# Performance work log

Measured on AMD Instinct MI355X. Metric: run time of the kernel, lower is better.

## Reference

```python
import jax, jax.numpy as jnp
import numpy as np

WS = 7        # window size
IMG = 56      # input resolution (H = W)
BATCH = 32    # image batch
DIM = 384
HEADS = 12
HEAD_DIM = DIM // HEADS
N = WS * WS                      # tokens per window = 49
NW = (IMG // WS) * (IMG // WS)   # windows per image = 64
B_ = BATCH * NW                  # 2048
TBL = (2 * WS - 1) ** 2          # 169


def _rel_index(ws):
    # standard Swin relative position index, values in [0, (2ws-1)^2)
    coords = np.stack(np.meshgrid(np.arange(ws), np.arange(ws), indexing='ij'))
    coords = coords.reshape(2, -1)                       # (2, N)
    rel = coords[:, :, None] - coords[:, None, :]        # (2, N, N)
    rel = rel.transpose(1, 2, 0).astype(np.int64).copy()
    rel[:, :, 0] += ws - 1
    rel[:, :, 1] += ws - 1
    rel[:, :, 0] *= 2 * ws - 1
    return rel.sum(-1)                                   # (N, N)


def _shift_mask(H, W, ws, shift):
    # shifted-window attention mask, (nW, N, N) with 0 / -100
    img = np.zeros((H, W))
    cnt = 0
    for hs in (slice(0, -ws), slice(-ws, -shift), slice(-shift, None)):
        for wsl in (slice(0, -ws), slice(-ws, -shift), slice(-shift, None)):
            img[hs, wsl] = cnt
            cnt += 1
    win = img.reshape(H // ws, ws, W // ws, ws).transpose(0, 2, 1, 3).reshape(-1, ws * ws)
    diff = win[:, None, :] - win[:, :, None]
    return np.where(diff != 0, -100.0, 0.0).astype(np.float32)


def setup_inputs() -> dict:
    key = jax.random.key(0)
    ks = jax.random.split(key, 7)
    s = 0.02
    return {
        'x': jax.random.normal(ks[0], (B_, N, DIM), jnp.float32),
        'mask': jnp.asarray(_shift_mask(IMG, IMG, WS, WS // 2)),
        'rpe_indices': jnp.asarray(_rel_index(WS)),
        'qkv_w': jax.random.normal(ks[1], (3 * DIM, DIM), jnp.float32) * s,
        'qkv_b': jnp.zeros((3 * DIM,), jnp.float32),
        'proj_w': jax.random.normal(ks[2], (DIM, DIM), jnp.float32) * s,
        'proj_b': jnp.zeros((DIM,), jnp.float32),
        'q_rpe': jax.random.normal(ks[3], (HEADS, HEAD_DIM, TBL), jnp.float32) * s,
        'k_rpe': jax.random.normal(ks[4], (HEADS, HEAD_DIM, TBL), jnp.float32) * s,
        'v_rpe': jax.random.normal(ks[5], (HEADS, TBL, HEAD_DIM), jnp.float32) * s,
    }


def reference(x, mask, rpe_indices, qkv_w, qkv_b, proj_w, proj_b, q_rpe, k_rpe, v_rpe):
    B, n, C = x.shape
    h, hd = q_rpe.shape[0], q_rpe.shape[1]
    scale = hd ** -0.5

    qkv = x @ qkv_w.T + qkv_b                                   # (B, N, 3C)
    qkv = qkv.reshape(B, n, 3, h, hd).transpose(2, 0, 3, 1, 4)   # (3, B, h, N, hd)
    q, k, v = qkv[0] * scale, qkv[1], qkv[2]

    attn = jnp.einsum('bhid,bhjd->bhij', q, k)                   # (B, h, N, N)

    # Contextual q/k bias. The torch code does b_q.flatten(2)[:, :, rpe_indices]
    # with rpe_indices in [0, TBL): gathering from the flattened (N*TBL) axis with
    # indices < TBL selects row 0 of the N axis, i.e. b_q[:, :, 0, rpe_indices].
    # We compute only that row, which is mathematically identical.
    bq0 = jnp.einsum('bhd,hdt->bht', q[:, :, 0], q_rpe)          # (B, h, TBL)
    bk0 = jnp.einsum('bhd,hdt->bht', k[:, :, 0], k_rpe)          # (B, h, TBL)
    attn = attn + (bq0 + bk0)[:, :, rpe_indices]                 # gather -> (B, h, N, N)

    nW = mask.shape[0]
    attn = attn.reshape(B // nW, nW, h, n, n) + mask[None, :, None]
    attn = jax.nn.softmax(attn.reshape(B, h, n, n), axis=-1)

    # contextual v bias: w = v_rpe[:, rpe_indices] -> (h, N, N, hd)
    w = v_rpe[:, rpe_indices.reshape(-1)].reshape(h, n, n, hd)
    r_v = jnp.einsum('bhij,hijd->bihd', attn, w).reshape(B, n, C)

    out = jnp.einsum('bhij,bhjd->bihd', attn, v).reshape(B, n, C) + r_v
    out = out @ proj_w.T + proj_b
    return out, attn
```

## Files before the change

### kernel.cpp

```cpp
#include <hip/hip_runtime.h>


typedef unsigned int u32;
typedef unsigned short u16;
typedef __attribute__((ext_vector_type(8))) short bf16x8;
typedef __attribute__((ext_vector_type(4))) float f32x4;
typedef float f4a __attribute__((ext_vector_type(4), aligned(4)));

#define SCALE 0.17677669529663687f

__device__ __forceinline__ u16 f2b(float f) {
  union { float f; u32 u; } c; c.f = f;
  u32 u = c.u;
  return (u16)((u + 0x7FFFu + ((u >> 16) & 1u)) >> 16);
}
__device__ __forceinline__ float b2f(u16 s) {
  union { float f; u32 u; } c; c.u = ((u32)s) << 16;
  return c.f;
}
__device__ __forceinline__ u32 pk2(float lo, float hi) {
  return (u32)f2b(lo) | ((u32)f2b(hi) << 16);
}
__device__ __forceinline__ void async16(void* lds, const void* g) {
  __builtin_amdgcn_global_load_lds(
      (const __attribute__((address_space(1))) u32*)g,
      (__attribute__((address_space(3))) u32*)lds, 16, 0, 0);
}

__global__ __launch_bounds__(256) void k_prep(
    const float* __restrict__ qkv_w, const float* __restrict__ proj_w,
    const float* __restrict__ mask, const int* __restrict__ idx,
    u16* __restrict__ wqkvb, u16* __restrict__ wprojb, u16* __restrict__ mbi) {
  int bx = blockIdx.x, tid = threadIdx.x;
  if (bx < 432) {
    int i = bx * 256 + tid;
    float4 v = ((const float4*)qkv_w)[i];
    ushort4 o; o.x = f2b(v.x); o.y = f2b(v.y); o.z = f2b(v.z); o.w = f2b(v.w);
    ((ushort4*)wqkvb)[i] = o;
  } else if (bx < 576) {
    int i = (bx - 432) * 256 + tid;
    float4 v = ((const float4*)proj_w)[i];
    ushort4 o; o.x = f2b(v.x); o.y = f2b(v.y); o.z = f2b(v.z); o.w = f2b(v.w);
    ((ushort4*)wprojb)[i] = o;
  } else {
    int i = (bx - 576) * 256 + tid;
    if (i < 64 * 2401) {
      int p = i % 2401;
      mbi[i] = (u16)(idx[p] | ((mask[i] != 0.0f) ? 256 : 0));
    }
  }
}

__global__ __launch_bounds__(256) void k_qkv(
    const float* __restrict__ X, const u16* __restrict__ Bw,
    const float* __restrict__ bias, u16* __restrict__ outq) {
  int bx0 = blockIdx.x;
  int bx = (bx0 & 7) * 882 + (bx0 >> 3);
  int mt = bx / 9, nt = bx - mt * 9;
  size_t m0 = (size_t)mt * 128;
  int n0 = nt * 128;
  int tid = threadIdx.x;
  int w = tid >> 6, l = tid & 63;
  int wm = w >> 1, wn = w & 1;
  int lr = l & 15, lg = l >> 4;
  int rdo = (lg ^ ((lr >> 1) & 3)) << 3;

  __shared__ u16 At[4096];
  __shared__ u16 Bt[2][4096];

  f32x4 acc[4][4] = {};
  int row = tid >> 2;
  int c8 = (((tid & 3) ^ ((row >> 1) & 3)) << 3);
  const u16* gB  = Bw + (size_t)(n0 + row) * 384 + c8;
  const u16* gB2 = Bw + (size_t)(n0 + row + 64) * 384 + c8;
  const float* gX  = X + (m0 + row) * 384 + c8;
  const float* gX2 = X + (m0 + row + 64) * 384 + c8;

  float4 ar[2][4];
  async16(&Bt[0][tid * 8], gB);
  async16(&Bt[0][(256 + tid) * 8], gB2);
  ar[0][0] = *(const float4*)(gX);
  ar[0][1] = *(const float4*)(gX + 4);
  ar[0][2] = *(const float4*)(gX2);
  ar[0][3] = *(const float4*)(gX2 + 4);

#pragma unroll
  for (int t = 0; t < 12; ++t) {
    int cur = t & 1, nxt = cur ^ 1;
    int k1 = ((t < 11) ? (t + 1) : 11) * 32;
    async16(&Bt[nxt][tid * 8], gB + k1);
    async16(&Bt[nxt][(256 + tid) * 8], gB2 + k1);
    ar[nxt][0] = *(const float4*)(gX + k1);
    ar[nxt][1] = *(const float4*)(gX + k1 + 4);
    ar[nxt][2] = *(const float4*)(gX2 + k1);
    ar[nxt][3] = *(const float4*)(gX2 + k1 + 4);
    asm volatile("s_waitcnt vmcnt(6)" ::: "memory");
    u32 p0[4], p1[4];
    p0[0] = pk2(ar[cur][0].x, ar[cur][0].y);
    p0[1] = pk2(ar[cur][0].z, ar[cur][0].w);
    p0[2] = pk2(ar[cur][1].x, ar[cur][1].y);
    p0[3] = pk2(ar[cur][1].z, ar[cur][1].w);
    p1[0] = pk2(ar[cur][2].x, ar[cur][2].y);
    p1[1] = pk2(ar[cur][2].z, ar[cur][2].w);
    p1[2] = pk2(ar[cur][3].x, ar[cur][3].y);
    p1[3] = pk2(ar[cur][3].z, ar[cur][3].w);
    *(uint4*)&At[tid * 8] = *(uint4*)p0;
    *(uint4*)&At[(256 + tid) * 8] = *(uint4*)p1;
    asm volatile("s_waitcnt lgkmcnt(0)\n\ts_barrier" ::: "memory");
    bf16x8 af[4], bfr[4];
#pragma unroll
    for (int mi = 0; mi < 4; ++mi)
      af[mi] = *(const bf16x8*)&At[(wm * 64 + mi * 16 + lr) * 32 + rdo];
#pragma unroll
    for (int ni = 0; ni < 4; ++ni)
      bfr[ni] = *(const bf16x8*)&Bt[cur][(wn * 64 + ni * 16 + lr) * 32 + rdo];
#pragma unroll
    for (int mi = 0; mi < 4; ++mi)
#pragma unroll
      for (int ni = 0; ni < 4; ++ni)
        acc[mi][ni] = __builtin_amdgcn_mfma_f32_16x16x32_bf16(af[mi], bfr[ni], acc[mi][ni], 0, 0, 0);
    asm volatile("s_waitcnt lgkmcnt(0)\n\ts_barrier" ::: "memory");
  }
  int lgq = l >> 4;
#pragma unroll
  for (int ni = 0; ni < 4; ++ni) {
    int cc = n0 + wn * 64 + ni * 16 + lr;
    float bv = bias[cc];
    float sc = (cc < 384) ? SCALE : 1.0f;
#pragma unroll
    for (int mi = 0; mi < 4; ++mi)
#pragma unroll
      for (int r = 0; r < 4; ++r) {
        size_t rr = m0 + wm * 64 + mi * 16 + lgq * 4 + r;
        outq[rr * 1152 + cc] = f2b((acc[mi][ni][r] + bv) * sc);
      }
  }
}

__global__ __launch_bounds__(256) void k_bqk(
    const u16* __restrict__ qkv, const float* __restrict__ q_rpe,
    const float* __restrict__ k_rpe, float* __restrict__ bqk) {
  int bx = blockIdx.x;
  int mtile = bx / 12, h = bx % 12;
  int b0 = mtile * 64;
  int tid = threadIdx.x;
  int w = tid >> 6, l = tid & 63;
  int lr = l & 15, g = l >> 4;

  __shared__ __align__(16) u16 At[64 * 64];
  __shared__ __align__(16) u16 Bt[192 * 64];

  {
    int m = tid >> 2;
#pragma unroll
    for (int rnd = 0; rnd < 2; ++rnd) {
      int c = (tid & 3) + rnd * 4;
      const u16* src = qkv + (size_t)(b0 + m) * 56448 + h * 32 +
                       ((c < 4) ? c * 8 : 384 + (c - 4) * 8);
      bf16x8 v = *(const bf16x8*)src;
      int byte = (m * 128 + c * 16) ^ ((m & 7) << 4);
      *(bf16x8*)((char*)At + byte) = v;
    }
  }
  if (tid < 192) {
    int t = tid;
#pragma unroll
    for (int c = 0; c < 8; ++c) {
      u16 pk[8];
#pragma unroll
      for (int e = 0; e < 8; ++e) {
        int d = (c & 3) * 8 + e;
        float v = 0.f;
        if (t < 169)
          v = (c < 4) ? q_rpe[(h * 32 + d) * 169 + t]
                      : k_rpe[(h * 32 + d) * 169 + t];
        pk[e] = f2b(v);
      }
      int byte = (t * 128 + c * 16) ^ ((t & 7) << 4);
      *(bf16x8*)((char*)Bt + byte) = *(bf16x8*)pk;
    }
  }
  __syncthreads();

  f32x4 acc[12] = {};
  bf16x8 af[2];
#pragma unroll
  for (int ks = 0; ks < 2; ++ks) {
    int row = w * 16 + lr;
    af[ks] = *(const bf16x8*)((const char*)At +
              ((row * 128 + ks * 64 + g * 16) ^ ((row & 7) << 4)));
  }
#pragma unroll
  for (int nt = 0; nt < 12; ++nt) {
#pragma unroll
    for (int ks = 0; ks < 2; ++ks) {
      int t = nt * 16 + lr;
      bf16x8 bf = *(const bf16x8*)((const char*)Bt +
                   ((t * 128 + ks * 64 + g * 16) ^ ((t & 7) << 4)));
      acc[nt] = __builtin_amdgcn_mfma_f32_16x16x32_bf16(af[ks], bf, acc[nt], 0, 0, 0);
    }
  }
#pragma unroll
  for (int nt = 0; nt < 12; ++nt) {
    int t = nt * 16 + lr;
    if (t < 169) {
#pragma unroll
      for (int r = 0; r < 4; ++r) {
        int b = b0 + w * 16 + g * 4 + r;
        bqk[((size_t)b * 12 + h) * 169 + t] = acc[nt][r];
      }
    }
  }
}

__global__ __launch_bounds__(256) void k_attn(
    const u16* __restrict__ qkv, const float* __restrict__ bqkG,
    const u16* __restrict__ mbi,
    float* __restrict__ attn, u16* __restrict__ o1) {
  int blk0 = blockIdx.x;
  int blk = (blk0 & 7) * 768 + (blk0 >> 3);
  int b = blk / 3, hg = blk % 3;
  int tid = threadIdx.x, w = tid >> 6, l = tid & 63;
  int h = hg * 4 + w;
  int lr = l & 15, g = l >> 4;

  __shared__ __align__(16) char LDSR[32160];
  u16* mbiL = (u16*)LDSR;
  float* bqkL = (float*)(LDSR + 4832);
  char* Uw = LDSR + 7584 + w * 6144;
  char* vt = Uw;
  char* slab = Uw + 4096;
  float* aw = (float*)Uw;

  const u16* qbase = qkv + (size_t)b * 49 * 1152 + h * 32;
  const u16* kbase = qbase + 384;
  const u16* vbase = qbase + 768;

  {
    const u16* mrow = mbi + (size_t)(b & 63) * 2401;
    for (int p = tid; p < 2401; p += 256) mbiL[p] = mrow[p];
  }
  {
    int jr = (l < 49) ? l : 48;
    const u16* vr = vbase + (size_t)jr * 1152;
#pragma unroll
    for (int d0 = 0; d0 < 4; ++d0) {
      uint4 vv = *(const uint4*)(vr + d0 * 8);
      u16 el[8];
      *(uint4*)el = vv;
#pragma unroll
      for (int e = 0; e < 8; ++e) {
        int d = d0 * 8 + e;
        int byte = d * 128 + ((l * 2) ^ ((d & 7) << 4));
        *(u16*)(vt + byte) = el[e];
      }
    }
  }
  {
    const float* bg = bqkG + ((size_t)b * 12 + h) * 169;
#pragma unroll
    for (int t0 = 0; t0 < 192; t0 += 64) {
      int t = t0 + l;
      if (t < 169) bqkL[w * 172 + t] = bg[t];
    }
  }

  bf16x8 qf[4], kf[4];
#pragma unroll
  for (int t = 0; t < 4; ++t) {
    int qi = t * 16 + lr;
    int qir = (qi < 49) ? qi : 48;
    qf[t] = *(const bf16x8*)(qbase + (size_t)qir * 1152 + g * 8);
    kf[t] = *(const bf16x8*)(kbase + (size_t)qir * 1152 + g * 8);
  }

  f32x4 S[4][4] = {};
#pragma unroll
  for (int mt = 0; mt < 4; ++mt)
#pragma unroll
    for (int nt = 0; nt < 4; ++nt)
      S[mt][nt] = __builtin_amdgcn_mfma_f32_16x16x32_bf16(kf[mt], qf[nt], S[mt][nt], 0, 0, 0);

  __syncthreads();

#pragma unroll
  for (int nt = 0; nt < 4; ++nt) {
    int qi = nt * 16 + lr;
#pragma unroll
    for (int mt = 0; mt < 4; ++mt)
#pragma unroll
      for (int r = 0; r < 4; ++r) {
        int kj = mt * 16 + g * 4 + r;
        float s = S[mt][nt][r];
        if (qi < 49 && kj < 49) {
          u16 t = mbiL[qi * 49 + kj];
          s += bqkL[w * 172 + (t & 255)] - 100.f * (float)(t >> 8);
        } else {
          s = -1e9f;
        }
        S[mt][nt][r] = s;
      }
  }

  float rinv[4];
#pragma unroll
  for (int nt = 0; nt < 4; ++nt) {
    float m = -1e30f;
#pragma unroll
    for (int mt = 0; mt < 4; ++mt)
#pragma unroll
      for (int r = 0; r < 4; ++r) m = fmaxf(m, S[mt][nt][r]);
    m = fmaxf(m, __shfl_xor(m, 16, 64));
    m = fmaxf(m, __shfl_xor(m, 32, 64));
    float sum = 0.f;
#pragma unroll
    for (int mt = 0; mt < 4; ++mt)
#pragma unroll
      for (int r = 0; r < 4; ++r) {
        float e = __expf(S[mt][nt][r] - m);
        S[mt][nt][r] = e;
        sum += e;
      }
    sum += __shfl_xor(sum, 16, 64);
    sum += __shfl_xor(sum, 32, 64);
    rinv[nt] = 1.f / sum;
  }

  bf16x8 va[2][2];
#pragma unroll
  for (int ks = 0; ks < 2; ++ks)
#pragma unroll
    for (int mtd = 0; mtd < 2; ++mtd) {
      int d = mtd * 16 + lr;
      int byte = d * 128 + ((ks * 64 + g * 16) ^ ((d & 7) << 4));
      va[ks][mtd] = *(const bf16x8*)(vt + byte);
    }

  f32x4 O[2][4] = {};
  int swz = (lr & 7) << 4;
#pragma unroll
  for (int nt = 0; nt < 4; ++nt) {
#pragma unroll
    for (int mt = 0; mt < 4; ++mt) {
      u32 w0 = (u32)f2b(S[mt][nt][0]) | ((u32)f2b(S[mt][nt][1]) << 16);
      u32 w1 = (u32)f2b(S[mt][nt][2]) | ((u32)f2b(S[mt][nt][3]) << 16);
      int off = (lr * 128 + mt * 32 + g * 8) ^ swz;
      uint2 pk = {w0, w1};
      *(uint2*)(slab + off) = pk;
    }
    bf16x8 pb0 = *(const bf16x8*)(slab + ((lr * 128 + g * 16) ^ swz));
    bf16x8 pb1 = *(const bf16x8*)(slab + ((lr * 128 + 64 + g * 16) ^ swz));
#pragma unroll
    for (int mtd = 0; mtd < 2; ++mtd) {
      O[mtd][nt] = __builtin_amdgcn_mfma_f32_16x16x32_bf16(va[0][mtd], pb0, O[mtd][nt], 0, 0, 0);
      O[mtd][nt] = __builtin_amdgcn_mfma_f32_16x16x32_bf16(va[1][mtd], pb1, O[mtd][nt], 0, 0, 0);
    }
  }

  {
    u16* ob = o1 + (size_t)b * 49 * 384 + h * 32;
#pragma unroll
    for (int nti = 0; nti < 4; ++nti) {
      int i = nti * 16 + lr;
      if (i < 49) {
        float riv = rinv[nti];
#pragma unroll
        for (int mtd = 0; mtd < 2; ++mtd) {
          u32 w0 = (u32)f2b(O[mtd][nti][0] * riv) | ((u32)f2b(O[mtd][nti][1] * riv) << 16);
          u32 w1 = (u32)f2b(O[mtd][nti][2] * riv) | ((u32)f2b(O[mtd][nti][3] * riv) << 16);
          uint2 pk = {w0, w1};
          *(uint2*)&ob[(size_t)i * 384 + mtd * 16 + g * 4] = pk;
        }
      }
    }
  }

  asm volatile("s_waitcnt lgkmcnt(0)" ::: "memory");
  float* ao = attn + (size_t)(b * 12 + h) * 2401;
#pragma unroll
  for (int nt = 0; nt < 4; ++nt) {
    int qi = nt * 16 + lr;
    if (qi < 49) {
      float riv = rinv[nt];
#pragma unroll
      for (int mt = 0; mt < 4; ++mt)
#pragma unroll
        for (int r = 0; r < 4; ++r) {
          int kj = mt * 16 + g * 4 + r;
          if (kj < 49) aw[lr * 49 + kj] = S[mt][nt][r] * riv;
        }
    }
    asm volatile("s_waitcnt lgkmcnt(0)" ::: "memory");
    int lim = (nt < 3) ? 784 : 49;
#pragma unroll
    for (int it = 0; it < 13; ++it) {
      int p = l + it * 64;
      if (p < lim) ao[nt * 784 + p] = aw[p];
    }
    asm volatile("s_waitcnt lgkmcnt(0)" ::: "memory");
  }
}

__global__ __launch_bounds__(256) void k_rv(
    const float* __restrict__ attn, const int* __restrict__ idx,
    const float* __restrict__ v_rpe, u16* __restrict__ o1) {
  int bx = blockIdx.x;
  int bc = bx & 7;
  int hi = bx >> 3;
  int i = hi % 49, h = hi / 49;
  int b0 = bc * 256;
  int tid = threadIdx.x;
  int w = tid >> 6, l = tid & 63;
  int lr = l & 15, g = l >> 4;

  __shared__ __align__(16) u16 wT[32 * 64];

  if (tid < 196) {
    int j = tid >> 2, d0 = (tid & 3) * 8;
    const float* vr = v_rpe + ((size_t)h * 169 + idx[i * 49 + j]) * 32 + d0;
    float4 a = *(const float4*)vr;
    float4 bvv = *(const float4*)(vr + 4);
    float el[8] = {a.x, a.y, a.z, a.w, bvv.x, bvv.y, bvv.z, bvv.w};
#pragma unroll
    for (int e = 0; e < 8; ++e) {
      int d = d0 + e;
      int byte = (d * 128 + j * 2) ^ ((d & 7) << 4);
      *(u16*)((char*)wT + byte) = f2b(el[e]);
    }
  } else {
    int t = tid - 196;
    int j = 49 + (t >> 2), d0 = (t & 3) * 8;
#pragma unroll
    for (int e = 0; e < 8; ++e) {
      int d = d0 + e;
      int byte = (d * 128 + j * 2) ^ ((d & 7) << 4);
      *(u16*)((char*)wT + byte) = 0;
    }
  }
  __syncthreads();

  f32x4 acc[2][4] = {};
#pragma unroll
  for (int ks = 0; ks < 2; ++ks) {
    bf16x8 af[2];
#pragma unroll
    for (int mt = 0; mt < 2; ++mt) {
      int d = mt * 16 + lr;
      int byte = (d * 128 + ks * 64 + g * 16) ^ ((d & 7) << 4);
      af[mt] = *(const bf16x8*)((const char*)wT + byte);
    }
    int j0 = ks * 32 + g * 8;
#pragma unroll
    for (int nt = 0; nt < 4; ++nt) {
      int bl = w * 64 + nt * 16 + lr;
      const float* ar = attn + ((size_t)(b0 + bl) * 12 + h) * 2401 +
                        (size_t)i * 49 + j0;
      f4a v0 = *(const f4a*)ar;
      f4a v1 = *(const f4a*)(ar + 4);
      u16 pk[8];
#pragma unroll
      for (int e = 0; e < 8; ++e) {
        float vv = (e < 4) ? v0[e] : v1[e - 4];
        pk[e] = (j0 + e < 49) ? f2b(vv) : (u16)0;
      }
      bf16x8 bfr = *(bf16x8*)pk;
#pragma unroll
      for (int mt = 0; mt < 2; ++mt)
        acc[mt][nt] = __builtin_amdgcn_mfma_f32_16x16x32_bf16(af[mt], bfr, acc[mt][nt], 0, 0, 0);
    }
  }

#pragma unroll
  for (int nt = 0; nt < 4; ++nt) {
    int bl = w * 64 + nt * 16 + lr;
    u16* ob = o1 + ((size_t)(b0 + bl) * 49 + i) * 384 + h * 32;
#pragma unroll
    for (int mt = 0; mt < 2; ++mt) {
      int d = mt * 16 + g * 4;
      uint2 old = *(uint2*)&ob[d];
      uint2 nw;
      nw.x = (u32)f2b(b2f((u16)(old.x & 0xffff)) + acc[mt][nt][0]) |
             ((u32)f2b(b2f((u16)(old.x >> 16)) + acc[mt][nt][1]) << 16);
      nw.y = (u32)f2b(b2f((u16)(old.y & 0xffff)) + acc[mt][nt][2]) |
             ((u32)f2b(b2f((u16)(old.y >> 16)) + acc[mt][nt][3]) << 16);
      *(uint2*)&ob[d] = nw;
    }
  }
}

__global__ __launch_bounds__(256) void k_proj(
    const u16* __restrict__ A, const u16* __restrict__ Bw,
    const float* __restrict__ bias, float* __restrict__ out) {
  int bx0 = blockIdx.x;
  int bx = (bx0 & 7) * 294 + (bx0 >> 3);
  int mt = bx / 3, nt = bx - mt * 3;
  size_t m0 = (size_t)mt * 128;
  int n0 = nt * 128;
  int tid = threadIdx.x;
  int w = tid >> 6, l = tid & 63;
  int wm = w >> 1, wn = w & 1;
  int lr = l & 15, lg = l >> 4;
  int rdo = (lg ^ ((lr >> 1) & 3)) << 3;

  __shared__ u16 At[2][4096];
  __shared__ u16 Bt[2][4096];

  f32x4 acc[4][4] = {};
  int row = tid >> 2;
  int c8 = (((tid & 3) ^ ((row >> 1) & 3)) << 3);
  const u16* gA  = A + (m0 + row) * 384 + c8;
  const u16* gA2 = A + (m0 + row + 64) * 384 + c8;
  const u16* gB  = Bw + (size_t)(n0 + row) * 384 + c8;
  const u16* gB2 = Bw + (size_t)(n0 + row + 64) * 384 + c8;

  async16(&At[0][tid * 8], gA);
  async16(&At[0][(256 + tid) * 8], gA2);
  async16(&Bt[0][tid * 8], gB);
  async16(&Bt[0][(256 + tid) * 8], gB2);

#pragma unroll
  for (int t = 0; t < 12; ++t) {
    int cur = t & 1, nxt = cur ^ 1;
    int k1 = ((t < 11) ? (t + 1) : 11) * 32;
    async16(&At[nxt][tid * 8], gA + k1);
    async16(&At[nxt][(256 + tid) * 8], gA2 + k1);
    async16(&Bt[nxt][tid * 8], gB + k1);
    async16(&Bt[nxt][(256 + tid) * 8], gB2 + k1);
    asm volatile("s_waitcnt vmcnt(4)" ::: "memory");
    asm volatile("s_barrier" ::: "memory");
    bf16x8 af[4], bfr[4];
#pragma unroll
    for (int mi = 0; mi < 4; ++mi)
      af[mi] = *(const bf16x8*)&At[cur][(wm * 64 + mi * 16 + lr) * 32 + rdo];
#pragma unroll
    for (int ni = 0; ni < 4; ++ni)
      bfr[ni] = *(const bf16x8*)&Bt[cur][(wn * 64 + ni * 16 + lr) * 32 + rdo];
#pragma unroll
    for (int mi = 0; mi < 4; ++mi)
#pragma unroll
      for (int ni = 0; ni < 4; ++ni)
        acc[mi][ni] = __builtin_amdgcn_mfma_f32_16x16x32_bf16(af[mi], bfr[ni], acc[mi][ni], 0, 0, 0);
    asm volatile("s_waitcnt lgkmcnt(0)\n\ts_barrier" ::: "memory");
  }
  int lgq = l >> 4;
#pragma unroll
  for (int mi = 0; mi < 4; ++mi)
#pragma unroll
    for (int ni = 0; ni < 4; ++ni)
#pragma unroll
      for (int r = 0; r < 4; ++r) {
        int rr = wm * 64 + mi * 16 + lgq * 4 + r;
        int cc = wn * 64 + ni * 16 + lr;
        out[(m0 + rr) * 384 + (size_t)(n0 + cc)] = acc[mi][ni][r] + bias[n0 + cc];
      }
}

extern "C" void kernel_launch(void* const* d_in, const int* in_sizes, int n_in,
                              void* d_out, int out_size, void* d_ws, size_t ws_size,
                              hipStream_t stream) {
  const float* x      = (const float*)d_in[0];
  const float* mask   = (const float*)d_in[1];
  const int*   rpe    = (const int*)d_in[2];
  const float* qkv_w  = (const float*)d_in[3];
  const float* qkv_b  = (const float*)d_in[4];
  const float* proj_w = (const float*)d_in[5];
  const float* proj_b = (const float*)d_in[6];
  const float* q_rpe  = (const float*)d_in[7];
  const float* k_rpe  = (const float*)d_in[8];
  const float* v_rpe  = (const float*)d_in[9];

  float* out  = (float*)d_out;
  float* attn = out + (size_t)100352 * 384;

  char* ws = (char*)d_ws;
  u16*   qkvb   = (u16*)ws;
  u16*   wqkvb  = (u16*)(ws + 231211008);
  u16*   wprojb = (u16*)(ws + 232095744);
  u16*   mbi    = (u16*)(ws + 232390656);
  float* bqkG   = (float*)(ws + 232697984);
  u16*   o1     = (u16*)(ws + 249311360);

  k_prep<<<1177, 256, 0, stream>>>(qkv_w, proj_w, mask, rpe, wqkvb, wprojb, mbi);
  k_qkv<<<7056, 256, 0, stream>>>(x, wqkvb, qkv_b, qkvb);
  k_bqk<<<384, 256, 0, stream>>>(qkvb, q_rpe, k_rpe, bqkG);
  k_attn<<<6144, 256, 0, stream>>>(qkvb, bqkG, mbi, attn, o1);
  k_rv<<<4704, 256, 0, stream>>>(attn, rpe, v_rpe, o1);
  k_proj<<<2352, 256, 0, stream>>>(o1, wprojb, proj_b, out);
}
```

Measured before the change: 597.6 us.

## Load GEMM fragments directly from global memory, dropping LDS staging in qkv/proj

Both the QKV and projection GEMM kernels stop staging tiles through double-buffered LDS with async loads and barriers. Each wave now reads its MFMA A/B fragments straight from global memory, converting fp32 X to bf16 in registers for the QKV case. Launch bounds now request 4 blocks per CU. This removes LDS traffic and barrier stalls but loses inter-wave data sharing and software prefetch, so redundant global/L2 reads increase and load latency is less hidden.

```diff
diff --git a/kernel.cpp b/kernel.cpp
--- a/kernel.cpp
+++ b/kernel.cpp
@@ -51,7 +51,7 @@
   }
 }
 
-__global__ __launch_bounds__(256) void k_qkv(
+__global__ __launch_bounds__(256, 4) void k_qkv(
     const float* __restrict__ X, const u16* __restrict__ Bw,
     const float* __restrict__ bias, u16* __restrict__ outq) {
   int bx0 = blockIdx.x;
@@ -62,66 +62,36 @@
   int tid = threadIdx.x;
   int w = tid >> 6, l = tid & 63;
   int wm = w >> 1, wn = w & 1;
-  int lr = l & 15, lg = l >> 4;
-  int rdo = (lg ^ ((lr >> 1) & 3)) << 3;
-
-  __shared__ u16 At[4096];
-  __shared__ u16 Bt[2][4096];
+  int lr = l & 15, g = l >> 4;
 
   f32x4 acc[4][4] = {};
-  int row = tid >> 2;
-  int c8 = (((tid & 3) ^ ((row >> 1) & 3)) << 3);
-  const u16* gB  = Bw + (size_t)(n0 + row) * 384 + c8;
-  const u16* gB2 = Bw + (size_t)(n0 + row + 64) * 384 + c8;
-  const float* gX  = X + (m0 + row) * 384 + c8;
-  const float* gX2 = X + (m0 + row + 64) * 384 + c8;
-
-  float4 ar[2][4];
-  async16(&Bt[0][tid * 8], gB);
-  async16(&Bt[0][(256 + tid) * 8], gB2);
-  ar[0][0] = *(const float4*)(gX);
-  ar[0][1] = *(const float4*)(gX + 4);
-  ar[0][2] = *(const float4*)(gX2);
-  ar[0][3] = *(const float4*)(gX2 + 4);
+  const float* xA0 = X + (m0 + wm * 64 + lr) * 384 + g * 8;
+  const u16*   xB0 = Bw + (size_t)(n0 + wn * 64 + lr) * 384 + g * 8;
 
 #pragma unroll
   for (int t = 0; t < 12; ++t) {
-    int cur = t & 1, nxt = cur ^ 1;
-    int k1 = ((t < 11) ? (t + 1) : 11) * 32;
-    async16(&Bt[nxt][tid * 8], gB + k1);
-    async16(&Bt[nxt][(256 + tid) * 8], gB2 + k1);
-    ar[nxt][0] = *(const float4*)(gX + k1);
-    ar[nxt][1] = *(const float4*)(gX + k1 + 4);
-    ar[nxt][2] = *(const float4*)(gX2 + k1);
-    ar[nxt][3] = *(const float4*)(gX2 + k1 + 4);
-    asm volatile("s_waitcnt vmcnt(6)" ::: "memory");
-    u32 p0[4], p1[4];
-    p0[0] = pk2(ar[cur][0].x, ar[cur][0].y);
-    p0[1] = pk2(ar[cur][0].z, ar[cur][0].w);
-    p0[2] = pk2(ar[cur][1].x, ar[cur][1].y);
-    p0[3] = pk2(ar[cur][1].z, ar[cur][1].w);
-    p1[0] = pk2(ar[cur][2].x, ar[cur][2].y);
-    p1[1] = pk2(ar[cur][2].z, ar[cur][2].w);
-    p1[2] = pk2(ar[cur][3].x, ar[cur][3].y);
-    p1[3] = pk2(ar[cur][3].z, ar[cur][3].w);
-    *(uint4*)&At[tid * 8] = *(uint4*)p0;
-    *(uint4*)&At[(256 + tid) * 8] = *(uint4*)p1;
-    asm volatile("s_waitcnt lgkmcnt(0)\n\ts_barrier" ::: "memory");
+    int k0 = t * 32;
     bf16x8 af[4], bfr[4];
 #pragma unroll
-    for (int mi = 0; mi < 4; ++mi)
-      af[mi] = *(const bf16x8*)&At[(wm * 64 + mi * 16 + lr) * 32 + rdo];
+    for (int mi = 0; mi < 4; ++mi) {
+      const float* ap = xA0 + mi * (16 * 384) + k0;
+      float4 a0 = *(const float4*)ap;
+      float4 a1 = *(const float4*)(ap + 4);
+      u32 p[4];
+      p[0] = pk2(a0.x, a0.y); p[1] = pk2(a0.z, a0.w);
+      p[2] = pk2(a1.x, a1.y); p[3] = pk2(a1.z, a1.w);
+      af[mi] = *(bf16x8*)p;
+    }
 #pragma unroll
     for (int ni = 0; ni < 4; ++ni)
-      bfr[ni] = *(const bf16x8*)&Bt[cur][(wn * 64 + ni * 16 + lr) * 32 + rdo];
+      bfr[ni] = *(const bf16x8*)(xB0 + ni * (16 * 384) + k0);
 #pragma unroll
     for (int mi = 0; mi < 4; ++mi)
 #pragma unroll
       for (int ni = 0; ni < 4; ++ni)
         acc[mi][ni] = __builtin_amdgcn_mfma_f32_16x16x32_bf16(af[mi], bfr[ni], acc[mi][ni], 0, 0, 0);
-    asm volatile("s_waitcnt lgkmcnt(0)\n\ts_barrier" ::: "memory");
-  }
-  int lgq = l >> 4;
+  }
+
 #pragma unroll
   for (int ni = 0; ni < 4; ++ni) {
     int cc = n0 + wn * 64 + ni * 16 + lr;
@@ -131,7 +101,7 @@
     for (int mi = 0; mi < 4; ++mi)
 #pragma unroll
       for (int r = 0; r < 4; ++r) {
-        size_t rr = m0 + wm * 64 + mi * 16 + lgq * 4 + r;
+        size_t rr = m0 + wm * 64 + mi * 16 + g * 4 + r;
         outq[rr * 1152 + cc] = f2b((acc[mi][ni][r] + bv) * sc);
       }
   }
@@ -488,7 +458,7 @@
   }
 }
 
-__global__ __launch_bounds__(256) void k_proj(
+__global__ __launch_bounds__(256, 4) void k_proj(
     const u16* __restrict__ A, const u16* __restrict__ Bw,
     const float* __restrict__ bias, float* __restrict__ out) {
   int bx0 = blockIdx.x;
@@ -499,57 +469,36 @@
   int tid = threadIdx.x;
   int w = tid >> 6, l = tid & 63;
   int wm = w >> 1, wn = w & 1;
-  int lr = l & 15, lg = l >> 4;
-  int rdo = (lg ^ ((lr >> 1) & 3)) << 3;
-
-  __shared__ u16 At[2][4096];
-  __shared__ u16 Bt[2][4096];
+  int lr = l & 15, g = l >> 4;
 
   f32x4 acc[4][4] = {};
-  int row = tid >> 2;
-  int c8 = (((tid & 3) ^ ((row >> 1) & 3)) << 3);
-  const u16* gA  = A + (m0 + row) * 384 + c8;
-  const u16* gA2 = A + (m0 + row + 64) * 384 + c8;
-  const u16* gB  = Bw + (size_t)(n0 + row) * 384 + c8;
-  const u16* gB2 = Bw + (size_t)(n0 + row + 64) * 384 + c8;
-
-  async16(&At[0][tid * 8], gA);
-  async16(&At[0][(256 + tid) * 8], gA2);
-  async16(&Bt[0][tid * 8], gB);
-  async16(&Bt[0][(256 + tid) * 8], gB2);
+  const u16* pA0 = A + (m0 + wm * 64 + lr) * 384 + g * 8;
+  const u16* pB0 = Bw + (size_t)(n0 + wn * 64 + lr) * 384 + g * 8;
 
 #pragma unroll
   for (int t = 0; t < 12; ++t) {
-    int cur = t & 1, nxt = cur ^ 1;
-    int k1 = ((t < 11) ? (t + 1) : 11) * 32;
-    async16(&At[nxt][tid * 8], gA + k1);
-    async16(&At[nxt][(256 + tid) * 8], gA2 + k1);
-    async16(&Bt[nxt][tid * 8], gB + k1);
-    async16(&Bt[nxt][(256 + tid) * 8], gB2 + k1);
-    asm volatile("s_waitcnt vmcnt(4)" ::: "memory");
-    asm volatile("s_barrier" ::: "memory");
+    int k0 = t * 32;
     bf16x8 af[4], bfr[4];
 #pragma unroll
     for (int mi = 0; mi < 4; ++mi)
-      af[mi] = *(const bf16x8*)&At[cur][(wm * 64 + mi * 16 + lr) * 32 + rdo];
+      af[mi] = *(const bf16x8*)(pA0 + mi * (16 * 384) + k0);
 #pragma unroll
     for (int ni = 0; ni < 4; ++ni)
-      bfr[ni] = *(const bf16x8*)&Bt[cur][(wn * 64 + ni * 16 + lr) * 32 + rdo];
+      bfr[ni] = *(const bf16x8*)(pB0 + ni * (16 * 384) + k0);
 #pragma unroll
     for (int mi = 0; mi < 4; ++mi)
 #pragma unroll
       for (int ni = 0; ni < 4; ++ni)
         acc[mi][ni] = __builtin_amdgcn_mfma_f32_16x16x32_bf16(af[mi], bfr[ni], acc[mi][ni], 0, 0, 0);
-    asm volatile("s_waitcnt lgkmcnt(0)\n\ts_barrier" ::: "memory");
-  }
-  int lgq = l >> 4;
+  }
+
 #pragma unroll
   for (int mi = 0; mi < 4; ++mi)
 #pragma unroll
     for (int ni = 0; ni < 4; ++ni)
 #pragma unroll
       for (int r = 0; r < 4; ++r) {
-        int rr = wm * 64 + mi * 16 + lgq * 4 + r;
+        int rr = wm * 64 + mi * 16 + g * 4 + r;
         int cc = wn * 64 + ni * 16 + lr;
         out[(m0 + rr) * 384 + (size_t)(n0 + cc)] = acc[mi][ni][r] + bias[n0 + cc];
       }
```

Result: slower. 983.4 us (+64.6%).
